# Optimization experiments

Hardware: AMD Instinct MI355X
Metric: run time of the kernel (lower is better)

Reference implementation:

```python
import jax, jax.numpy as jnp
import numpy as np


def _pairwise_l2(set1, set2):
    # set1: [B, N, C], set2: [B, M, C] -> [B, N, M] Euclidean distances.
    # Equivalent to ||a - b||_2 computed via the expanded quadratic form,
    # avoiding the O(B*N*M*C) broadcasted-difference intermediate.
    sq1 = jnp.sum(set1 * set1, axis=-1)  # [B, N]
    sq2 = jnp.sum(set2 * set2, axis=-1)  # [B, M]
    inner = jnp.einsum('bnc,bmc->bnm', set1, set2)  # [B, N, M]
    d2 = sq1[:, :, None] + sq2[:, None, :] - 2.0 * inner
    return jnp.sqrt(jnp.maximum(d2, 0.0))


def reference(set1, set2):
    # mode == Hausdorff.average
    if set1.ndim == 2:
        set1 = set1[None]
    if set2.ndim == 2:
        set2 = set2[None]
    distances = _pairwise_l2(set1, set2)  # [B, N, M]
    term_1 = jnp.mean(jnp.min(distances, axis=2), axis=1)  # [B]
    term_2 = jnp.mean(jnp.min(distances, axis=1), axis=1)  # [B]
    res = term_1 + term_2
    if res.shape[0] == 1:
        res = jnp.squeeze(res, axis=0)
    return res


def setup_inputs() -> dict:
    key = jax.random.key(0)
    k1, k2 = jax.random.split(key)
    B, N, M, C = 8, 4096, 4096, 128
    set1 = jax.random.normal(k1, (B, N, C), dtype=jnp.float32)
    set2 = jax.random.normal(k2, (B, M, C), dtype=jnp.float32)
    return {"set1": set1, "set2": set2}
```

## Files before the change

### kernel.cpp

```cpp
#include <hip/hip_runtime.h>

#define B_ 8
#define N_ 4096
#define M_ 4096
#define C_ 128
#define BN_ (B_ * N_)
#define BM_ (B_ * M_)

typedef __attribute__((ext_vector_type(8))) short bf16x8;
typedef __attribute__((ext_vector_type(4))) float floatx4;
typedef __attribute__((ext_vector_type(8))) unsigned short ushort8;

__device__ __forceinline__ unsigned short f2bf(float x) {
    unsigned int u = __float_as_uint(x);
    u += 0x7FFFu + ((u >> 16) & 1u);
    return (unsigned short)(u >> 16);
}

__device__ __forceinline__ unsigned fkey(float f) {
    unsigned u = __float_as_uint(f);
    return u ^ (unsigned)(((int)u >> 31) | 0x80000000);
}
__device__ __forceinline__ float funkey(unsigned k) {
    unsigned u = (k & 0x80000000u) ? (k ^ 0x80000000u) : ~k;
    return __uint_as_float(u);
}

__device__ __forceinline__ void gl2lds16(const void* g, void* l) {
    __builtin_amdgcn_global_load_lds(
        (const __attribute__((address_space(1))) void*)g,
        (__attribute__((address_space(3))) void*)l, 16, 0, 0);
}

__global__ __launch_bounds__(256) void prep_kernel(
    const float* __restrict__ S1, const float* __restrict__ S2,
    float* __restrict__ norms, unsigned short* __restrict__ bfA,
    unsigned short* __restrict__ bfB, float* __restrict__ out) {
    const int lane = threadIdx.x & 63;
    const int w    = threadIdx.x >> 6;
    const int r4   = lane >> 4;
    const int g4   = lane & 15;

    #pragma unroll
    for (int step = 0; step < 4; ++step) {
        const int row = blockIdx.x * 64 + step * 16 + w * 4 + r4;

        const float* src = (row < BN_) ? S1 + (size_t)row * C_
                                       : S2 + (size_t)(row - BN_) * C_;
        float4 v0 = ((const float4*)src)[g4 * 2];
        float4 v1 = ((const float4*)src)[g4 * 2 + 1];

        float s = v0.x*v0.x + v0.y*v0.y + v0.z*v0.z + v0.w*v0.w
                + v1.x*v1.x + v1.y*v1.y + v1.z*v1.z + v1.w*v1.w;
        s += __shfl_xor(s, 1, 64);
        s += __shfl_xor(s, 2, 64);
        s += __shfl_xor(s, 4, 64);
        s += __shfl_xor(s, 8, 64);

        ushort8 o;
        o[0] = f2bf(v0.x); o[1] = f2bf(v0.y);
        o[2] = f2bf(v0.z); o[3] = f2bf(v0.w);
        o[4] = f2bf(v1.x); o[5] = f2bf(v1.y);
        o[6] = f2bf(v1.z); o[7] = f2bf(v1.w);

        unsigned short* dst = (row < BN_) ? bfA + (size_t)row * C_
                                          : bfB + (size_t)(row - BN_) * C_;
        *(ushort8*)&dst[(g4 ^ (row & 15)) * 8] = o;

        if (g4 == 0) norms[row] = -0.5f * s;
    }
    if (blockIdx.x == 0 && threadIdx.x < B_) out[threadIdx.x] = 0.f;
}

__global__ __launch_bounds__(256, 2) void hausdorff_mfma(
    const unsigned short* __restrict__ Abf, const unsigned short* __restrict__ Bbf,
    const float* __restrict__ ahalf_g, const float* __restrict__ bhalf_g,
    float* __restrict__ rowpart, float* __restrict__ colpart) {

    __shared__ unsigned short B_lds[2][64 * 128];
    __shared__ unsigned int colmax_u[1024][4];
    __shared__ float bhalf_lds[1024];

    const int b     = blockIdx.z;
    const int x     = blockIdx.x;
    const int panel = blockIdx.y;
    const int row0  = x * 256;
    const int tid   = threadIdx.x;
    const int lane  = tid & 63;
    const int w     = tid >> 6;
    const int lm    = lane & 15;
    const int quad  = lane >> 4;
    const int wrow  = w * 64;

    const unsigned short* Aws = Abf + ((size_t)b * N_ + row0 + wrow) * C_;
    const unsigned short* Bws = Bbf + ((size_t)b * M_ + (size_t)panel * 1024) * C_;

    {
        uint4 z; z.x = z.y = z.z = z.w = 0u;
        unsigned int* cm = &colmax_u[0][0];
        #pragma unroll
        for (int k = 0; k < 4; ++k)
            *(uint4*)&cm[tid * 16 + k * 4] = z;
    }

    gl2lds16(bhalf_g + (size_t)b * M_ + panel * 1024 + w * 256 + lane * 4,
             &bhalf_lds[w * 256]);

    bf16x8 af[4][4];
    #pragma unroll
    for (int i = 0; i < 4; ++i)
        #pragma unroll
        for (int c = 0; c < 4; ++c)
            af[i][c] = *(const bf16x8*)
                &Aws[(16 * i + lm) * 128 + (((c * 4 + quad) ^ lm) * 8)];

    float ha[16];
    #pragma unroll
    for (int i = 0; i < 4; ++i) {
        float4 t = *(const float4*)&ahalf_g[(size_t)b * N_ + row0 + wrow + 16 * i + 4 * quad];
        ha[4*i+0] = t.x; ha[4*i+1] = t.y; ha[4*i+2] = t.z; ha[4*i+3] = t.w;
    }

    float rv[16];
    #pragma unroll
    for (int v = 0; v < 16; ++v) rv[v] = -1e30f;

    #pragma unroll
    for (int k = 0; k < 4; ++k) {
        const int off = w * 2048 + k * 512;
        gl2lds16(Bws + off + lane * 8, &B_lds[0][off]);
    }

    for (int it = 0; it < 16; ++it) {
        const int cur = it & 1;
        __syncthreads();

        if (it < 15) {
            const unsigned short* Bt = Bws + (size_t)(it + 1) * 64 * C_;
            #pragma unroll
            for (int k = 0; k < 4; ++k) {
                const int off = w * 2048 + k * 512;
                gl2lds16(Bt + off + lane * 8, &B_lds[cur ^ 1][off]);
            }
        }

        float hb[4];
        #pragma unroll
        for (int j = 0; j < 4; ++j)
            hb[j] = bhalf_lds[it * 64 + 16 * j + lm];

        floatx4 acc[4][4];
        #pragma unroll
        for (int i = 0; i < 4; ++i)
            #pragma unroll
            for (int j = 0; j < 4; ++j)
                #pragma unroll
                for (int r = 0; r < 4; ++r)
                    acc[i][j][r] = ha[4 * i + r] + hb[j];

        #pragma unroll
        for (int h = 0; h < 2; ++h) {
            bf16x8 bfr[2][4];
            #pragma unroll
            for (int j2 = 0; j2 < 2; ++j2)
                #pragma unroll
                for (int c = 0; c < 4; ++c)
                    bfr[j2][c] = *(const bf16x8*)
                        &B_lds[cur][(16 * (2 * h + j2) + lm) * 128 +
                                    (((c * 4 + quad) ^ lm) * 8)];
            #pragma unroll
            for (int c = 0; c < 4; ++c)
                #pragma unroll
                for (int i = 0; i < 4; ++i)
                    #pragma unroll
                    for (int j2 = 0; j2 < 2; ++j2)
                        acc[i][2 * h + j2] = __builtin_amdgcn_mfma_f32_16x16x32_bf16(
                            af[i][c], bfr[j2][c], acc[i][2 * h + j2], 0, 0, 0);
        }

        #pragma unroll
        for (int i = 0; i < 4; ++i)
            #pragma unroll
            for (int r = 0; r < 4; ++r) {
                float m01 = fmaxf(acc[i][0][r], acc[i][1][r]);
                float m23 = fmaxf(acc[i][2][r], acc[i][3][r]);
                rv[4 * i + r] = fmaxf(rv[4 * i + r], fmaxf(m01, m23));
            }

        #pragma unroll
        for (int j = 0; j < 4; ++j) {
            float t0 = fmaxf(fmaxf(acc[0][j][0], acc[0][j][1]),
                             fmaxf(acc[0][j][2], acc[0][j][3]));
            float t1 = fmaxf(fmaxf(acc[1][j][0], acc[1][j][1]),
                             fmaxf(acc[1][j][2], acc[1][j][3]));
            float t2 = fmaxf(fmaxf(acc[2][j][0], acc[2][j][1]),
                             fmaxf(acc[2][j][2], acc[2][j][3]));
            float t3 = fmaxf(fmaxf(acc[3][j][0], acc[3][j][1]),
                             fmaxf(acc[3][j][2], acc[3][j][3]));
            float cv = fmaxf(fmaxf(t0, t1), fmaxf(t2, t3));
            atomicMax(&colmax_u[it * 64 + 16 * j + lm][quad], fkey(cv));
        }
    }

    #pragma unroll
    for (int s = 1; s < 16; s <<= 1)
        #pragma unroll
        for (int v = 0; v < 16; ++v)
            rv[v] = fmaxf(rv[v], __shfl_xor(rv[v], s, 64));
    if (lm == 0) {
        #pragma unroll
        for (int v = 0; v < 16; ++v)
            rowpart[((size_t)panel * B_ + b) * N_ + row0 + wrow +
                    16 * (v >> 2) + 4 * quad + (v & 3)] = rv[v];
    }

    __syncthreads();

    {
        const int c0 = tid * 4;
        float cout[4];
        #pragma unroll
        for (int cc = 0; cc < 4; ++cc) {
            uint4 q = *(const uint4*)&colmax_u[c0 + cc][0];
            unsigned k = max(max(q.x, q.y), max(q.z, q.w));
            cout[cc] = funkey(k);
        }
        *(float4*)&colpart[((size_t)x * B_ + b) * M_ + (size_t)panel * 1024 + c0] =
            *(float4*)cout;
    }
}

__global__ __launch_bounds__(256) void hausdorff_reduce(
    const float* __restrict__ rowpart, const float* __restrict__ colpart,
    float* __restrict__ out) {
    __shared__ float ws4[4];
    const int b    = blockIdx.x >> 3;
    const int part = blockIdx.x & 7;
    const int base = part * 512;
    float s = 0.f;
    for (int i = base + (int)threadIdx.x; i < base + 512; i += 256) {
        float ra = fmaxf(rowpart[((size_t)0 * B_ + b) * N_ + i],
                         rowpart[((size_t)1 * B_ + b) * N_ + i]);
        float rb = fmaxf(rowpart[((size_t)2 * B_ + b) * N_ + i],
                         rowpart[((size_t)3 * B_ + b) * N_ + i]);
        float rm = fmaxf(ra, rb);
        float ca = -1e30f, cb = -1e30f;
        #pragma unroll
        for (int xx = 0; xx < 16; xx += 2) {
            ca = fmaxf(ca, colpart[((size_t)xx * B_ + b) * M_ + i]);
            cb = fmaxf(cb, colpart[((size_t)(xx + 1) * B_ + b) * M_ + i]);
        }
        float cm = fmaxf(ca, cb);
        s += sqrtf(fmaxf(-2.f * rm, 0.f)) * (1.f / N_)
           + sqrtf(fmaxf(-2.f * cm, 0.f)) * (1.f / M_);
    }
    #pragma unroll
    for (int off = 32; off > 0; off >>= 1) s += __shfl_down(s, off, 64);
    if ((threadIdx.x & 63) == 0) ws4[threadIdx.x >> 6] = s;
    __syncthreads();
    if (threadIdx.x == 0)
        atomicAdd(&out[b], ws4[0] + ws4[1] + ws4[2] + ws4[3]);
}

extern "C" void kernel_launch(void* const* d_in, const int* in_sizes, int n_in,
                              void* d_out, int out_size, void* d_ws, size_t ws_size,
                              hipStream_t stream) {
    const float* s1 = (const float*)d_in[0];
    const float* s2 = (const float*)d_in[1];
    float* out = (float*)d_out;

    float* norms         = (float*)d_ws;
    unsigned short* bfA  = (unsigned short*)(norms + BN_ + BM_);
    unsigned short* bfB  = bfA + (size_t)BN_ * C_;
    float* rowpart       = (float*)(bfB + (size_t)BM_ * C_);
    float* colpart       = rowpart + (size_t)4 * B_ * N_;

    prep_kernel<<<(BN_ + BM_) / 64, 256, 0, stream>>>(
        s1, s2, norms, bfA, bfB, out);

    dim3 grid(N_ / 256, M_ / 1024, B_);
    hausdorff_mfma<<<grid, 256, 0, stream>>>(
        bfA, bfB, norms, norms + BN_, rowpart, colpart);

    hausdorff_reduce<<<B_ * 8, 256, 0, stream>>>(rowpart, colpart, out);
}
```

Before: 111.8 us.

## Prepack B into MFMA fragment layout and load directly from global to registers

The prep kernel now writes set2's bf16 data in a pre-swizzled fragment order, so each lane can fetch its MFMA B-operand with coalesced 16-byte global loads. The main kernel drops the double-buffered LDS staging of B and its per-tile barriers, and instead register-double-buffers one 16-column group at a time while computing 4x1 MFMA tiles. This removes LDS traffic and synchronisation, at the cost of more exposed global/L2 latency and more colmax atomics per column group.

```diff
diff --git a/kernel.cpp b/kernel.cpp
--- a/kernel.cpp
+++ b/kernel.cpp
@@ -63,21 +63,71 @@
         o[4] = f2bf(v1.x); o[5] = f2bf(v1.y);
         o[6] = f2bf(v1.z); o[7] = f2bf(v1.w);
 
-        unsigned short* dst = (row < BN_) ? bfA + (size_t)row * C_
-                                          : bfB + (size_t)(row - BN_) * C_;
-        *(ushort8*)&dst[(g4 ^ (row & 15)) * 8] = o;
+        if (row < BN_) {
+            unsigned short* dst = bfA + (size_t)row * C_;
+            *(ushort8*)&dst[(g4 ^ (row & 15)) * 8] = o;
+        } else {
+            const int rB   = row - BN_;
+            const int bb   = rB >> 12;
+            const int colb = rB & 4095;
+            unsigned short* dst = bfB + (size_t)bb * (M_ * C_)
+                                + (size_t)(colb >> 4) * 2048
+                                + (g4 >> 2) * 512
+                                + (((g4 & 3) * 16) + (colb & 15)) * 8;
+            *(ushort8*)dst = o;
+        }
 
         if (g4 == 0) norms[row] = -0.5f * s;
     }
     if (blockIdx.x == 0 && threadIdx.x < B_) out[threadIdx.x] = 0.f;
 }
 
+
+#define LOADB(dst_, g_)                                                       \
+  do {                                                                        \
+    _Pragma("unroll")                                                         \
+    for (int c_ = 0; c_ < 4; ++c_)                                            \
+        dst_[c_] = *(const bf16x8*)&Bp[(size_t)(g_) * 2048 + c_ * 512 + lane * 8]; \
+  } while (0)
+
+#define COMPUTE(bf_, g_)                                                      \
+  do {                                                                        \
+    const int gg_ = (g_);                                                     \
+    const float hb_ = bhalf_lds[gg_ * 16 + lm];                               \
+    floatx4 acc_[4];                                                          \
+    _Pragma("unroll")                                                         \
+    for (int i_ = 0; i_ < 4; ++i_)                                            \
+      _Pragma("unroll")                                                       \
+      for (int r_ = 0; r_ < 4; ++r_)                                          \
+          acc_[i_][r_] = ha[4 * i_ + r_] + hb_;                               \
+    _Pragma("unroll")                                                         \
+    for (int c_ = 0; c_ < 4; ++c_)                                            \
+      _Pragma("unroll")                                                       \
+      for (int i_ = 0; i_ < 4; ++i_)                                          \
+          acc_[i_] = __builtin_amdgcn_mfma_f32_16x16x32_bf16(                 \
+              af[i_][c_], bf_[c_], acc_[i_], 0, 0, 0);                        \
+    _Pragma("unroll")                                                         \
+    for (int i_ = 0; i_ < 4; ++i_)                                            \
+      _Pragma("unroll")                                                       \
+      for (int r_ = 0; r_ < 4; ++r_)                                          \
+          rv[4 * i_ + r_] = fmaxf(rv[4 * i_ + r_], acc_[i_][r_]);             \
+    float t0_ = fmaxf(fmaxf(acc_[0][0], acc_[0][1]),                          \
+                      fmaxf(acc_[0][2], acc_[0][3]));                         \
+    float t1_ = fmaxf(fmaxf(acc_[1][0], acc_[1][1]),                          \
+                      fmaxf(acc_[1][2], acc_[1][3]));                         \
+    float t2_ = fmaxf(fmaxf(acc_[2][0], acc_[2][1]),                          \
+                      fmaxf(acc_[2][2], acc_[2][3]));                         \
+    float t3_ = fmaxf(fmaxf(acc_[3][0], acc_[3][1]),                          \
+                      fmaxf(acc_[3][2], acc_[3][3]));                         \
+    float cv_ = fmaxf(fmaxf(t0_, t1_), fmaxf(t2_, t3_));                      \
+    atomicMax(&colmax_u[gg_ * 16 + lm][quad], fkey(cv_));                     \
+  } while (0)
+
 __global__ __launch_bounds__(256, 2) void hausdorff_mfma(
-    const unsigned short* __restrict__ Abf, const unsigned short* __restrict__ Bbf,
+    const unsigned short* __restrict__ Abf, const unsigned short* __restrict__ Bfr,
     const float* __restrict__ ahalf_g, const float* __restrict__ bhalf_g,
     float* __restrict__ rowpart, float* __restrict__ colpart) {
 
-    __shared__ unsigned short B_lds[2][64 * 128];
     __shared__ unsigned int colmax_u[1024][4];
     __shared__ float bhalf_lds[1024];
 
@@ -93,7 +143,8 @@
     const int wrow  = w * 64;
 
     const unsigned short* Aws = Abf + ((size_t)b * N_ + row0 + wrow) * C_;
-    const unsigned short* Bws = Bbf + ((size_t)b * M_ + (size_t)panel * 1024) * C_;
+    const unsigned short* Bp  = Bfr + (size_t)b * (M_ * C_)
+                              + (size_t)panel * 64 * 2048;
 
     {
         uint4 z; z.x = z.y = z.z = z.w = 0u;
@@ -125,81 +176,15 @@
     #pragma unroll
     for (int v = 0; v < 16; ++v) rv[v] = -1e30f;
 
-    #pragma unroll
-    for (int k = 0; k < 4; ++k) {
-        const int off = w * 2048 + k * 512;
-        gl2lds16(Bws + off + lane * 8, &B_lds[0][off]);
-    }
-
-    for (int it = 0; it < 16; ++it) {
-        const int cur = it & 1;
-        __syncthreads();
-
-        if (it < 15) {
-            const unsigned short* Bt = Bws + (size_t)(it + 1) * 64 * C_;
-            #pragma unroll
-            for (int k = 0; k < 4; ++k) {
-                const int off = w * 2048 + k * 512;
-                gl2lds16(Bt + off + lane * 8, &B_lds[cur ^ 1][off]);
-            }
-        }
-
-        float hb[4];
-        #pragma unroll
-        for (int j = 0; j < 4; ++j)
-            hb[j] = bhalf_lds[it * 64 + 16 * j + lm];
-
-        floatx4 acc[4][4];
-        #pragma unroll
-        for (int i = 0; i < 4; ++i)
-            #pragma unroll
-            for (int j = 0; j < 4; ++j)
-                #pragma unroll
-                for (int r = 0; r < 4; ++r)
-                    acc[i][j][r] = ha[4 * i + r] + hb[j];
-
-        #pragma unroll
-        for (int h = 0; h < 2; ++h) {
-            bf16x8 bfr[2][4];
-            #pragma unroll
-            for (int j2 = 0; j2 < 2; ++j2)
-                #pragma unroll
-                for (int c = 0; c < 4; ++c)
-                    bfr[j2][c] = *(const bf16x8*)
-                        &B_lds[cur][(16 * (2 * h + j2) + lm) * 128 +
-                                    (((c * 4 + quad) ^ lm) * 8)];
-            #pragma unroll
-            for (int c = 0; c < 4; ++c)
-                #pragma unroll
-                for (int i = 0; i < 4; ++i)
-                    #pragma unroll
-                    for (int j2 = 0; j2 < 2; ++j2)
-                        acc[i][2 * h + j2] = __builtin_amdgcn_mfma_f32_16x16x32_bf16(
-                            af[i][c], bfr[j2][c], acc[i][2 * h + j2], 0, 0, 0);
-        }
-
-        #pragma unroll
-        for (int i = 0; i < 4; ++i)
-            #pragma unroll
-            for (int r = 0; r < 4; ++r) {
-                float m01 = fmaxf(acc[i][0][r], acc[i][1][r]);
-                float m23 = fmaxf(acc[i][2][r], acc[i][3][r]);
-                rv[4 * i + r] = fmaxf(rv[4 * i + r], fmaxf(m01, m23));
-            }
-
-        #pragma unroll
-        for (int j = 0; j < 4; ++j) {
-            float t0 = fmaxf(fmaxf(acc[0][j][0], acc[0][j][1]),
-                             fmaxf(acc[0][j][2], acc[0][j][3]));
-            float t1 = fmaxf(fmaxf(acc[1][j][0], acc[1][j][1]),
-                             fmaxf(acc[1][j][2], acc[1][j][3]));
-            float t2 = fmaxf(fmaxf(acc[2][j][0], acc[2][j][1]),
-                             fmaxf(acc[2][j][2], acc[2][j][3]));
-            float t3 = fmaxf(fmaxf(acc[3][j][0], acc[3][j][1]),
-                             fmaxf(acc[3][j][2], acc[3][j][3]));
-            float cv = fmaxf(fmaxf(t0, t1), fmaxf(t2, t3));
-            atomicMax(&colmax_u[it * 64 + 16 * j + lm][quad], fkey(cv));
-        }
+    __syncthreads();
+
+    bf16x8 bfrA[4], bfrB[4];
+    LOADB(bfrA, 0);
+    for (int g = 0; g < 64; g += 2) {
+        LOADB(bfrB, g + 1);
+        COMPUTE(bfrA, g);
+        if (g + 2 < 64) LOADB(bfrA, g + 2);
+        COMPUTE(bfrB, g + 1);
     }
 
     #pragma unroll
```

Measured after the change: 113.7 us. About the same (+1.7%).

## Fuse fp32-to-bf16 conversion and norm computation into the MFMA distance kernel

Applied to the files above, without the earlier changes.

Drops the separate prep kernel. The main kernel now reads fp32 inputs directly, converts them to bf16 in registers and computes the squared norms on the fly. The B tiles are prefetched into registers and written to LDS after the compute of each iteration, replacing async global-to-LDS loads, and the sync moves to the end of each iteration. This removes a kernel launch and the round trip of the bf16 and norm buffers through global memory. In exchange it reads twice as many bytes per tile in fp32, repeats the conversion for every panel and row-block, and adds register pressure that could lower occupancy.

```diff
diff --git a/kernel.cpp b/kernel.cpp
--- a/kernel.cpp
+++ b/kernel.cpp
@@ -17,6 +17,13 @@
     return (unsigned short)(u >> 16);
 }
 
+__device__ __forceinline__ bf16x8 pack8(float4 a, float4 b) {
+    ushort8 o;
+    o[0] = f2bf(a.x); o[1] = f2bf(a.y); o[2] = f2bf(a.z); o[3] = f2bf(a.w);
+    o[4] = f2bf(b.x); o[5] = f2bf(b.y); o[6] = f2bf(b.z); o[7] = f2bf(b.w);
+    return *(bf16x8*)&o;
+}
+
 __device__ __forceinline__ unsigned fkey(float f) {
     unsigned u = __float_as_uint(f);
     return u ^ (unsigned)(((int)u >> 31) | 0x80000000);
@@ -26,60 +33,15 @@
     return __uint_as_float(u);
 }
 
-__device__ __forceinline__ void gl2lds16(const void* g, void* l) {
-    __builtin_amdgcn_global_load_lds(
-        (const __attribute__((address_space(1))) void*)g,
-        (__attribute__((address_space(3))) void*)l, 16, 0, 0);
-}
-
-__global__ __launch_bounds__(256) void prep_kernel(
+__global__ __launch_bounds__(256, 2) void hausdorff_fused(
     const float* __restrict__ S1, const float* __restrict__ S2,
-    float* __restrict__ norms, unsigned short* __restrict__ bfA,
-    unsigned short* __restrict__ bfB, float* __restrict__ out) {
-    const int lane = threadIdx.x & 63;
-    const int w    = threadIdx.x >> 6;
-    const int r4   = lane >> 4;
-    const int g4   = lane & 15;
-
-    #pragma unroll
-    for (int step = 0; step < 4; ++step) {
-        const int row = blockIdx.x * 64 + step * 16 + w * 4 + r4;
-
-        const float* src = (row < BN_) ? S1 + (size_t)row * C_
-                                       : S2 + (size_t)(row - BN_) * C_;
-        float4 v0 = ((const float4*)src)[g4 * 2];
-        float4 v1 = ((const float4*)src)[g4 * 2 + 1];
-
-        float s = v0.x*v0.x + v0.y*v0.y + v0.z*v0.z + v0.w*v0.w
-                + v1.x*v1.x + v1.y*v1.y + v1.z*v1.z + v1.w*v1.w;
-        s += __shfl_xor(s, 1, 64);
-        s += __shfl_xor(s, 2, 64);
-        s += __shfl_xor(s, 4, 64);
-        s += __shfl_xor(s, 8, 64);
-
-        ushort8 o;
-        o[0] = f2bf(v0.x); o[1] = f2bf(v0.y);
-        o[2] = f2bf(v0.z); o[3] = f2bf(v0.w);
-        o[4] = f2bf(v1.x); o[5] = f2bf(v1.y);
-        o[6] = f2bf(v1.z); o[7] = f2bf(v1.w);
-
-        unsigned short* dst = (row < BN_) ? bfA + (size_t)row * C_
-                                          : bfB + (size_t)(row - BN_) * C_;
-        *(ushort8*)&dst[(g4 ^ (row & 15)) * 8] = o;
-
-        if (g4 == 0) norms[row] = -0.5f * s;
-    }
-    if (blockIdx.x == 0 && threadIdx.x < B_) out[threadIdx.x] = 0.f;
-}
-
-__global__ __launch_bounds__(256, 2) void hausdorff_mfma(
-    const unsigned short* __restrict__ Abf, const unsigned short* __restrict__ Bbf,
-    const float* __restrict__ ahalf_g, const float* __restrict__ bhalf_g,
-    float* __restrict__ rowpart, float* __restrict__ colpart) {
+    float* __restrict__ rowpart, float* __restrict__ colpart,
+    float* __restrict__ out) {
 
     __shared__ unsigned short B_lds[2][64 * 128];
     __shared__ unsigned int colmax_u[1024][4];
-    __shared__ float bhalf_lds[1024];
+    __shared__ float bhalf_t[2][64];
+    __shared__ float ascr[256];
 
     const int b     = blockIdx.z;
     const int x     = blockIdx.x;
@@ -92,8 +54,7 @@
     const int quad  = lane >> 4;
     const int wrow  = w * 64;
 
-    const unsigned short* Aws = Abf + ((size_t)b * N_ + row0 + wrow) * C_;
-    const unsigned short* Bws = Bbf + ((size_t)b * M_ + (size_t)panel * 1024) * C_;
+    if (x == 0 && panel == 0 && tid == 0) out[b] = 0.f;
 
     {
         uint4 z; z.x = z.y = z.z = z.w = 0u;
@@ -103,51 +64,84 @@
             *(uint4*)&cm[tid * 16 + k * 4] = z;
     }
 
-    gl2lds16(bhalf_g + (size_t)b * M_ + panel * 1024 + w * 256 + lane * 4,
-             &bhalf_lds[w * 256]);
-
+    const float* As = S1 + ((size_t)b * N_ + row0 + wrow) * C_;
     bf16x8 af[4][4];
     #pragma unroll
-    for (int i = 0; i < 4; ++i)
-        #pragma unroll
-        for (int c = 0; c < 4; ++c)
-            af[i][c] = *(const bf16x8*)
-                &Aws[(16 * i + lm) * 128 + (((c * 4 + quad) ^ lm) * 8)];
+    for (int i = 0; i < 4; ++i) {
+        float ss = 0.f;
+        #pragma unroll
+        for (int c = 0; c < 4; ++c) {
+            const float* p = As + (size_t)(16 * i + lm) * C_ + c * 32 + quad * 8;
+            float4 u0 = *(const float4*)p;
+            float4 u1 = *(const float4*)(p + 4);
+            ss += u0.x*u0.x + u0.y*u0.y + u0.z*u0.z + u0.w*u0.w
+                + u1.x*u1.x + u1.y*u1.y + u1.z*u1.z + u1.w*u1.w;
+            af[i][c] = pack8(u0, u1);
+        }
+        ss += __shfl_xor(ss, 16, 64);
+        ss += __shfl_xor(ss, 32, 64);
+        if (quad == 0) ascr[wrow + 16 * i + lm] = -0.5f * ss;
+    }
+
+    const float* Bs = S2 + ((size_t)b * M_ + (size_t)panel * 1024) * C_;
+    const int scol = tid >> 2;
+    const int sk4  = tid & 3;
+
+#define STAGE_LOAD(q_, it_)                                                   \
+    do {                                                                      \
+        const float* sp_ = Bs + (size_t)((it_) * 64 + scol) * C_ + sk4 * 32;  \
+        _Pragma("unroll")                                                     \
+        for (int jj_ = 0; jj_ < 8; ++jj_)                                     \
+            q_[jj_] = *(const float4*)(sp_ + jj_ * 4);                        \
+    } while (0)
+
+#define STAGE_WRITE(q_, buf_)                                                 \
+    do {                                                                      \
+        float ss_ = 0.f;                                                      \
+        _Pragma("unroll")                                                     \
+        for (int jj_ = 0; jj_ < 8; ++jj_)                                     \
+            ss_ += q_[jj_].x*q_[jj_].x + q_[jj_].y*q_[jj_].y                  \
+                 + q_[jj_].z*q_[jj_].z + q_[jj_].w*q_[jj_].w;                 \
+        ss_ += __shfl_xor(ss_, 1, 64);                                        \
+        ss_ += __shfl_xor(ss_, 2, 64);                                        \
+        if (sk4 == 0) bhalf_t[buf_][scol] = -0.5f * ss_;                      \
+        _Pragma("unroll")                                                     \
+        for (int jj_ = 0; jj_ < 4; ++jj_) {                                   \
+            bf16x8 o_ = pack8(q_[2 * jj_], q_[2 * jj_ + 1]);                  \
+            const int g_ = sk4 * 4 + jj_;                                     \
+            *(bf16x8*)&B_lds[buf_][scol * 128 + ((g_ ^ (scol & 15)) * 8)] = o_; \
+        }                                                                     \
+    } while (0)
+
+    {
+        float4 q[8];
+        STAGE_LOAD(q, 0);
+        STAGE_WRITE(q, 0);
+    }
+
+    __syncthreads();
 
     float ha[16];
     #pragma unroll
     for (int i = 0; i < 4; ++i) {
-        float4 t = *(const float4*)&ahalf_g[(size_t)b * N_ + row0 + wrow + 16 * i + 4 * quad];
+        float4 t = *(const float4*)&ascr[wrow + 16 * i + 4 * quad];
         ha[4*i+0] = t.x; ha[4*i+1] = t.y; ha[4*i+2] = t.z; ha[4*i+3] = t.w;
     }
 
     float rv[16];
     #pragma unroll
     for (int v = 0; v < 16; ++v) rv[v] = -1e30f;
-
-    #pragma unroll
-    for (int k = 0; k < 4; ++k) {
-        const int off = w * 2048 + k * 512;
-        gl2lds16(Bws + off + lane * 8, &B_lds[0][off]);
-    }
 
     for (int it = 0; it < 16; ++it) {
         const int cur = it & 1;
-        __syncthreads();
-
-        if (it < 15) {
-            const unsigned short* Bt = Bws + (size_t)(it + 1) * 64 * C_;
-            #pragma unroll
-            for (int k = 0; k < 4; ++k) {
-                const int off = w * 2048 + k * 512;
-                gl2lds16(Bt + off + lane * 8, &B_lds[cur ^ 1][off]);
-            }
-        }
+
+        float4 q[8];
+        if (it < 15) STAGE_LOAD(q, it + 1);
 
         float hb[4];
         #pragma unroll
         for (int j = 0; j < 4; ++j)
-            hb[j] = bhalf_lds[it * 64 + 16 * j + lm];
+            hb[j] = bhalf_t[cur][16 * j + lm];
 
         floatx4 acc[4][4];
         #pragma unroll
@@ -200,6 +194,10 @@
             float cv = fmaxf(fmaxf(t0, t1), fmaxf(t2, t3));
             atomicMax(&colmax_u[it * 64 + 16 * j + lm][quad], fkey(cv));
         }
+
+        if (it < 15) STAGE_WRITE(q, cur ^ 1);
+
+        __syncthreads();
     }
 
     #pragma unroll
@@ -214,7 +212,6 @@
                     16 * (v >> 2) + 4 * quad + (v & 3)] = rv[v];
     }
 
-    __syncthreads();
 
     {
         const int c0 = tid * 4;
@@ -269,18 +266,11 @@
     const float* s2 = (const float*)d_in[1];
     float* out = (float*)d_out;
 
-    float* norms         = (float*)d_ws;
-    unsigned short* bfA  = (unsigned short*)(norms + BN_ + BM_);
-    unsigned short* bfB  = bfA + (size_t)BN_ * C_;
-    float* rowpart       = (float*)(bfB + (size_t)BM_ * C_);
-    float* colpart       = rowpart + (size_t)4 * B_ * N_;
-
-    prep_kernel<<<(BN_ + BM_) / 64, 256, 0, stream>>>(
-        s1, s2, norms, bfA, bfB, out);
+    float* rowpart = (float*)d_ws;
+    float* colpart = rowpart + (size_t)4 * B_ * N_;
 
     dim3 grid(N_ / 256, M_ / 1024, B_);
-    hausdorff_mfma<<<grid, 256, 0, stream>>>(
-        bfA, bfB, norms, norms + BN_, rowpart, colpart);
+    hausdorff_fused<<<grid, 256, 0, stream>>>(s1, s2, rowpart, colpart, out);
 
     hausdorff_reduce<<<B_ * 8, 256, 0, stream>>>(rowpart, colpart, out);
 }
```

New measurement: 145.7 us. +30.3%, slower.

## Fuse set1 bf16 conversion into MFMA kernel and fold reduction via last-block counter

Applied to the files above, without the earlier changes.

The prep kernel now converts and normalises only set2. Each MFMA block loads its fp32 set1 rows directly, computes their norms and packs them to bf16 in registers. The separate reduce kernel is replaced by an atomic per-batch counter, so the last of the 64 blocks for a batch does the final row/column reduction and writes the output. This removes one launch and the bf16 set1 round trip through memory. In exchange, set1 rows are read in fp32 (twice the bytes) and each set1 tile is re-read by all 4 panels, and the final reduction runs serially in one block per batch.

```diff
diff --git a/kernel.cpp b/kernel.cpp
--- a/kernel.cpp
+++ b/kernel.cpp
@@ -17,6 +17,13 @@
     return (unsigned short)(u >> 16);
 }
 
+__device__ __forceinline__ bf16x8 pack8(float4 a, float4 b) {
+    ushort8 o;
+    o[0] = f2bf(a.x); o[1] = f2bf(a.y); o[2] = f2bf(a.z); o[3] = f2bf(a.w);
+    o[4] = f2bf(b.x); o[5] = f2bf(b.y); o[6] = f2bf(b.z); o[7] = f2bf(b.w);
+    return *(bf16x8*)&o;
+}
+
 __device__ __forceinline__ unsigned fkey(float f) {
     unsigned u = __float_as_uint(f);
     return u ^ (unsigned)(((int)u >> 31) | 0x80000000);
@@ -32,10 +39,9 @@
         (__attribute__((address_space(3))) void*)l, 16, 0, 0);
 }
 
-__global__ __launch_bounds__(256) void prep_kernel(
-    const float* __restrict__ S1, const float* __restrict__ S2,
-    float* __restrict__ norms, unsigned short* __restrict__ bfA,
-    unsigned short* __restrict__ bfB, float* __restrict__ out) {
+__global__ __launch_bounds__(256) void prep_b(
+    const float* __restrict__ S2, float* __restrict__ norms,
+    unsigned short* __restrict__ bfB, unsigned int* __restrict__ cnt) {
     const int lane = threadIdx.x & 63;
     const int w    = threadIdx.x >> 6;
     const int r4   = lane >> 4;
@@ -45,8 +51,7 @@
     for (int step = 0; step < 4; ++step) {
         const int row = blockIdx.x * 64 + step * 16 + w * 4 + r4;
 
-        const float* src = (row < BN_) ? S1 + (size_t)row * C_
-                                       : S2 + (size_t)(row - BN_) * C_;
+        const float* src = S2 + (size_t)row * C_;
         float4 v0 = ((const float4*)src)[g4 * 2];
         float4 v1 = ((const float4*)src)[g4 * 2 + 1];
 
@@ -57,29 +62,26 @@
         s += __shfl_xor(s, 4, 64);
         s += __shfl_xor(s, 8, 64);
 
-        ushort8 o;
-        o[0] = f2bf(v0.x); o[1] = f2bf(v0.y);
-        o[2] = f2bf(v0.z); o[3] = f2bf(v0.w);
-        o[4] = f2bf(v1.x); o[5] = f2bf(v1.y);
-        o[6] = f2bf(v1.z); o[7] = f2bf(v1.w);
-
-        unsigned short* dst = (row < BN_) ? bfA + (size_t)row * C_
-                                          : bfB + (size_t)(row - BN_) * C_;
-        *(ushort8*)&dst[(g4 ^ (row & 15)) * 8] = o;
+        unsigned short* dst = bfB + (size_t)row * C_;
+        *(bf16x8*)&dst[(g4 ^ (row & 15)) * 8] = pack8(v0, v1);
 
         if (g4 == 0) norms[row] = -0.5f * s;
     }
-    if (blockIdx.x == 0 && threadIdx.x < B_) out[threadIdx.x] = 0.f;
+    if (blockIdx.x == 0 && threadIdx.x < B_) cnt[threadIdx.x] = 0u;
 }
 
 __global__ __launch_bounds__(256, 2) void hausdorff_mfma(
-    const unsigned short* __restrict__ Abf, const unsigned short* __restrict__ Bbf,
-    const float* __restrict__ ahalf_g, const float* __restrict__ bhalf_g,
-    float* __restrict__ rowpart, float* __restrict__ colpart) {
+    const float* __restrict__ S1, const unsigned short* __restrict__ Bbf,
+    const float* __restrict__ bhalf_g, float* __restrict__ rowpart,
+    float* __restrict__ colpart, unsigned int* __restrict__ cnt,
+    float* __restrict__ out) {
 
     __shared__ unsigned short B_lds[2][64 * 128];
     __shared__ unsigned int colmax_u[1024][4];
     __shared__ float bhalf_lds[1024];
+    __shared__ float ascr[256];
+    __shared__ float ws4[4];
+    __shared__ int islast;
 
     const int b     = blockIdx.z;
     const int x     = blockIdx.x;
@@ -92,7 +94,6 @@
     const int quad  = lane >> 4;
     const int wrow  = w * 64;
 
-    const unsigned short* Aws = Abf + ((size_t)b * N_ + row0 + wrow) * C_;
     const unsigned short* Bws = Bbf + ((size_t)b * M_ + (size_t)panel * 1024) * C_;
 
     {
@@ -106,24 +107,24 @@
     gl2lds16(bhalf_g + (size_t)b * M_ + panel * 1024 + w * 256 + lane * 4,
              &bhalf_lds[w * 256]);
 
+    const float* As = S1 + ((size_t)b * N_ + row0 + wrow) * C_;
     bf16x8 af[4][4];
     #pragma unroll
-    for (int i = 0; i < 4; ++i)
-        #pragma unroll
-        for (int c = 0; c < 4; ++c)
-            af[i][c] = *(const bf16x8*)
-                &Aws[(16 * i + lm) * 128 + (((c * 4 + quad) ^ lm) * 8)];
-
-    float ha[16];
-    #pragma unroll
     for (int i = 0; i < 4; ++i) {
-        float4 t = *(const float4*)&ahalf_g[(size_t)b * N_ + row0 + wrow + 16 * i + 4 * quad];
-        ha[4*i+0] = t.x; ha[4*i+1] = t.y; ha[4*i+2] = t.z; ha[4*i+3] = t.w;
-    }
-
-    float rv[16];
-    #pragma unroll
-    for (int v = 0; v < 16; ++v) rv[v] = -1e30f;
+        float ss = 0.f;
+        #pragma unroll
+        for (int c = 0; c < 4; ++c) {
+            const float* p = As + (size_t)(16 * i + lm) * C_ + c * 32 + quad * 8;
+            float4 u0 = *(const float4*)p;
+            float4 u1 = *(const float4*)(p + 4);
+            ss += u0.x*u0.x + u0.y*u0.y + u0.z*u0.z + u0.w*u0.w
+                + u1.x*u1.x + u1.y*u1.y + u1.z*u1.z + u1.w*u1.w;
+            af[i][c] = pack8(u0, u1);
+        }
+        ss += __shfl_xor(ss, 16, 64);
+        ss += __shfl_xor(ss, 32, 64);
+        if (quad == 0) ascr[wrow + 16 * i + lm] = -0.5f * ss;
+    }
 
     #pragma unroll
     for (int k = 0; k < 4; ++k) {
@@ -131,9 +132,22 @@
         gl2lds16(Bws + off + lane * 8, &B_lds[0][off]);
     }
 
+    __syncthreads();
+
+    float ha[16];
+    #pragma unroll
+    for (int i = 0; i < 4; ++i) {
+        float4 t = *(const float4*)&ascr[wrow + 16 * i + 4 * quad];
+        ha[4*i+0] = t.x; ha[4*i+1] = t.y; ha[4*i+2] = t.z; ha[4*i+3] = t.w;
+    }
+
+    float rv[16];
+    #pragma unroll
+    for (int v = 0; v < 16; ++v) rv[v] = -1e30f;
+
     for (int it = 0; it < 16; ++it) {
         const int cur = it & 1;
-        __syncthreads();
+        if (it) __syncthreads();
 
         if (it < 15) {
             const unsigned short* Bt = Bws + (size_t)(it + 1) * 64 * C_;
@@ -228,17 +242,15 @@
         *(float4*)&colpart[((size_t)x * B_ + b) * M_ + (size_t)panel * 1024 + c0] =
             *(float4*)cout;
     }
-}
-
-__global__ __launch_bounds__(256) void hausdorff_reduce(
-    const float* __restrict__ rowpart, const float* __restrict__ colpart,
-    float* __restrict__ out) {
-    __shared__ float ws4[4];
-    const int b    = blockIdx.x >> 3;
-    const int part = blockIdx.x & 7;
-    const int base = part * 512;
+
+    __threadfence();
+    if (tid == 0) islast = (atomicAdd(&cnt[b], 1u) == 63u);
+    __syncthreads();
+    if (!islast) return;
+    __threadfence();
+
     float s = 0.f;
-    for (int i = base + (int)threadIdx.x; i < base + 512; i += 256) {
+    for (int i = tid; i < N_; i += 256) {
         float ra = fmaxf(rowpart[((size_t)0 * B_ + b) * N_ + i],
                          rowpart[((size_t)1 * B_ + b) * N_ + i]);
         float rb = fmaxf(rowpart[((size_t)2 * B_ + b) * N_ + i],
@@ -256,10 +268,9 @@
     }
     #pragma unroll
     for (int off = 32; off > 0; off >>= 1) s += __shfl_down(s, off, 64);
-    if ((threadIdx.x & 63) == 0) ws4[threadIdx.x >> 6] = s;
-    __syncthreads();
-    if (threadIdx.x == 0)
-        atomicAdd(&out[b], ws4[0] + ws4[1] + ws4[2] + ws4[3]);
+    if ((tid & 63) == 0) ws4[tid >> 6] = s;
+    __syncthreads();
+    if (tid == 0) out[b] = ws4[0] + ws4[1] + ws4[2] + ws4[3];
 }
 
 extern "C" void kernel_launch(void* const* d_in, const int* in_sizes, int n_in,
@@ -269,18 +280,15 @@
     const float* s2 = (const float*)d_in[1];
     float* out = (float*)d_out;
 
-    float* norms         = (float*)d_ws;
-    unsigned short* bfA  = (unsigned short*)(norms + BN_ + BM_);
-    unsigned short* bfB  = bfA + (size_t)BN_ * C_;
+    float* bnorms        = (float*)d_ws;
+    unsigned short* bfB  = (unsigned short*)(bnorms + BM_);
     float* rowpart       = (float*)(bfB + (size_t)BM_ * C_);
     float* colpart       = rowpart + (size_t)4 * B_ * N_;
-
-    prep_kernel<<<(BN_ + BM_) / 64, 256, 0, stream>>>(
-        s1, s2, norms, bfA, bfB, out);
+    unsigned int* cnt    = (unsigned int*)(colpart + (size_t)16 * B_ * M_);
+
+    prep_b<<<BM_ / 64, 256, 0, stream>>>(s2, bnorms, bfB, cnt);
 
     dim3 grid(N_ / 256, M_ / 1024, B_);
     hausdorff_mfma<<<grid, 256, 0, stream>>>(
-        bfA, bfB, norms, norms + BN_, rowpart, colpart);
-
-    hausdorff_reduce<<<B_ * 8, 256, 0, stream>>>(rowpart, colpart, out);
-}
+        s1, bfB, bnorms, rowpart, colpart, cnt, out);
+}
```

After: 163.2 us. 46.1% more time.
